# Kernel optimization log

Hardware: AMD Instinct MI355X
Metric: run time of the kernel (lower is better)

The kernel has to match this reference:

```python
import jax, jax.numpy as jnp
import numpy as np
import math

H = 8          # num_heads
DV = 1024      # dim_V
LN_EPS = 1e-5


def _layernorm(x, g, b):
    mu = jnp.mean(x, axis=-1, keepdims=True)
    var = jnp.mean(jnp.square(x - mu), axis=-1, keepdims=True)
    return (x - mu) * jax.lax.rsqrt(var + LN_EPS) * g + b


def setup_inputs() -> dict:
    key = jax.random.key(0)
    ks = jax.random.split(key, 12)
    B, NQ, NK, DQ, DK = 4, 2048, 2048, 1024, 1024
    s = 0.02
    return {
        "Q": jax.random.normal(ks[0], (B, NQ, DQ), jnp.float32),
        "K": jax.random.normal(ks[1], (B, NK, DK), jnp.float32),
        "Wq": jax.random.normal(ks[2], (DV, DQ), jnp.float32) * s,
        "bq": jnp.zeros((DV,), jnp.float32),
        "Wk": jax.random.normal(ks[3], (DV, DK), jnp.float32) * s,
        "bk": jnp.zeros((DV,), jnp.float32),
        "Wv": jax.random.normal(ks[4], (DV, DK), jnp.float32) * s,
        "bv": jnp.zeros((DV,), jnp.float32),
        "Wo": jax.random.normal(ks[5], (DV, DV), jnp.float32) * s,
        "bo": jnp.zeros((DV,), jnp.float32),
        "g0": jnp.ones((DV,), jnp.float32),
        "b0": jnp.zeros((DV,), jnp.float32),
        "g1": jnp.ones((DV,), jnp.float32),
        "b1": jnp.zeros((DV,), jnp.float32),
    }


def reference(Q, K, Wq, bq, Wk, bk, Wv, bv, Wo, bo, g0, b0, g1, b1):
    B, NQ, _ = Q.shape
    NK = K.shape[1]
    d = DV // H  # per-head dim
    # projections
    q = (Q @ Wq.T + bq).reshape(B, NQ, H, d)
    k = (K @ Wk.T + bk).reshape(B, NK, H, d)
    v = (K @ Wv.T + bv).reshape(B, NK, H, d)
    # attention per head (split along feature dim == head split in torch code)
    logits = jnp.einsum('bqhd,bkhd->bhqk', q, k) / math.sqrt(d)
    A = jax.nn.softmax(logits, axis=-1)
    o = q + jnp.einsum('bhqk,bkhd->bqhd', A, v)  # residual with projected Q
    O = o.reshape(B, NQ, DV)
    O = _layernorm(O, g0, b0)
    O = O + jax.nn.relu(O @ Wo.T + bo)
    O = _layernorm(O, g1, b1)
    return O
```

## Files before the change

### kernel.cpp

```cpp
#include <hip/hip_runtime.h>
#include <hip/hip_bf16.h>

typedef __bf16 bf16_t;
typedef __bf16 bf16x8 __attribute__((ext_vector_type(8)));
typedef __bf16 bf16x4 __attribute__((ext_vector_type(4)));
typedef float f32x4 __attribute__((ext_vector_type(4)));

#define B_DIM 4
#define NQ 2048
#define NK 2048
#define DMODEL 1024
#define NH 8
#define DHEAD 128

#define AS1 __attribute__((address_space(1)))
#define AS3 __attribute__((address_space(3)))

__device__ __forceinline__ void gl_lds16(const void* g, void* l) {
    __builtin_amdgcn_global_load_lds((const AS1 void*)g, (AS3 void*)l, 16, 0, 0);
}

struct CvtArgs {
    const float* s[6];
    bf16_t* d[6];
    int n[6];
};

__global__ __launch_bounds__(256) void cvt_k(CvtArgs a) {
    const int p = blockIdx.y;
    const float* s = a.s[p];
    bf16_t* d = a.d[p];
    const int n = a.n[p];
    const int stride = gridDim.x * 256 * 8;
    for (int i = (blockIdx.x * 256 + threadIdx.x) * 8; i < n; i += stride) {
        float4 x0 = *(const float4*)(s + i);
        float4 x1 = *(const float4*)(s + i + 4);
        bf16x8 o = {(bf16_t)x0.x, (bf16_t)x0.y, (bf16_t)x0.z, (bf16_t)x0.w,
                    (bf16_t)x1.x, (bf16_t)x1.y, (bf16_t)x1.z, (bf16_t)x1.w};
        *(bf16x8*)(d + i) = o;
    }
}

__global__ __launch_bounds__(256) void proj_k(
    const bf16_t* Qc, const bf16_t* Kc,
    const bf16_t* Wqc, const bf16_t* Wkc, const bf16_t* Wvc,
    const float* bq, const float* bk, const float* bv,
    bf16_t* qbb, bf16_t* kbb, bf16_t* vT)
{
    const int K = DMODEL, N = DMODEL;
    const int z = blockIdx.z;
    const bf16_t* A  = (z == 0) ? Qc : Kc;
    const bf16_t* Bw = (z == 0) ? Wqc : (z == 1) ? Wkc : Wvc;
    const float* bias = (z == 0) ? bq : (z == 1) ? bk : bv;
    bf16_t* Cb = (z == 0) ? qbb : (z == 1) ? kbb : vT;

    const int tid  = threadIdx.x;
    const int lane = tid & 63;
    const int wv   = tid >> 6;
    const int l16  = lane & 15;
    const int quad = (lane >> 4) & 3;
    const int kc4  = lane >> 4;
    const int wr   = wv >> 1, wc = wv & 1;
    const int rowBase = blockIdx.y * 128;
    const int colBase = blockIdx.x * 128;

    __shared__ bf16_t sA[4096];
    __shared__ bf16_t sB[4096];

    const bf16_t* gA = A + (size_t)(rowBase + wv * 32 + l16) * K + kc4 * 8;
    const bf16_t* gB = Bw + (size_t)(colBase + wv * 32 + l16) * K + kc4 * 8;
    bf16_t* lA0 = &sA[(wv * 2) * 512];
    bf16_t* lA1 = &sA[(wv * 2 + 1) * 512];
    bf16_t* lB0 = &sB[(wv * 2) * 512];
    bf16_t* lB1 = &sB[(wv * 2 + 1) * 512];

    const f32x4 fz = {0.f, 0.f, 0.f, 0.f};
    f32x4 acc[4][4];
#pragma unroll
    for (int i = 0; i < 4; i++)
#pragma unroll
        for (int j = 0; j < 4; j++) acc[i][j] = fz;

    for (int k0 = 0; k0 < K; k0 += 32) {
        gl_lds16(gA, lA0);
        gl_lds16(gA + (size_t)16 * K, lA1);
        gl_lds16(gB, lB0);
        gl_lds16(gB + (size_t)16 * K, lB1);
        gA += 32; gB += 32;
        __syncthreads();

        bf16x8 aF[4], bF[4];
#pragma unroll
        for (int mi = 0; mi < 4; mi++)
            aF[mi] = *(const bf16x8*)(&sA[(wr * 4 + mi) * 512 + (quad * 16 + l16) * 8]);
#pragma unroll
        for (int ni = 0; ni < 4; ni++)
            bF[ni] = *(const bf16x8*)(&sB[(wc * 4 + ni) * 512 + (quad * 16 + l16) * 8]);
#pragma unroll
        for (int mi = 0; mi < 4; mi++)
#pragma unroll
            for (int ni = 0; ni < 4; ni++)
                acc[mi][ni] = __builtin_amdgcn_mfma_f32_16x16x32_bf16(
                    aF[mi], bF[ni], acc[mi][ni], 0, 0, 0);
        __syncthreads();
    }

#pragma unroll
    for (int mi = 0; mi < 4; mi++) {
#pragma unroll
        for (int ni = 0; ni < 4; ni++) {
            int row0 = rowBase + wr * 64 + mi * 16 + quad * 4;
            int col  = colBase + wc * 64 + ni * 16 + l16;
            float bvv = bias[col];
            if (z != 2) {
#pragma unroll
                for (int r = 0; r < 4; r++)
                    Cb[(size_t)(row0 + r) * N + col] = (bf16_t)(acc[mi][ni][r] + bvv);
            } else {
                int b  = row0 >> 11;
                int n0 = row0 & 2047;
                int hh = col >> 7;
                int dd = col & 127;
                bf16x4 p = {(bf16_t)(acc[mi][ni][0] + bvv), (bf16_t)(acc[mi][ni][1] + bvv),
                            (bf16_t)(acc[mi][ni][2] + bvv), (bf16_t)(acc[mi][ni][3] + bvv)};
                *(bf16x4*)(Cb + (size_t)((b * NH + hh) * DHEAD + dd) * NK + n0) = p;
            }
        }
    }
}

__global__ __launch_bounds__(256) void gemm_wo(
    const bf16_t* __restrict__ A, const bf16_t* __restrict__ Bw,
    const float* __restrict__ bias, const float* resid, float* Cf, int M, int N, int K)
{
    const int tid  = threadIdx.x;
    const int lane = tid & 63;
    const int wv   = tid >> 6;
    const int l16  = lane & 15;
    const int quad = (lane >> 4) & 3;
    const int kc4  = lane >> 4;
    const int wr   = wv >> 1, wc = wv & 1;
    const int rowBase = blockIdx.y * 128;
    const int colBase = blockIdx.x * 128;

    __shared__ bf16_t sA[4096];
    __shared__ bf16_t sB[4096];

    const bf16_t* gA = A + (size_t)(rowBase + wv * 32 + l16) * K + kc4 * 8;
    const bf16_t* gB = Bw + (size_t)(colBase + wv * 32 + l16) * K + kc4 * 8;
    bf16_t* lA0 = &sA[(wv * 2) * 512];
    bf16_t* lA1 = &sA[(wv * 2 + 1) * 512];
    bf16_t* lB0 = &sB[(wv * 2) * 512];
    bf16_t* lB1 = &sB[(wv * 2 + 1) * 512];

    const f32x4 fz = {0.f, 0.f, 0.f, 0.f};
    f32x4 acc[4][4];
#pragma unroll
    for (int i = 0; i < 4; i++)
#pragma unroll
        for (int j = 0; j < 4; j++) acc[i][j] = fz;

    for (int k0 = 0; k0 < K; k0 += 32) {
        gl_lds16(gA, lA0);
        gl_lds16(gA + (size_t)16 * K, lA1);
        gl_lds16(gB, lB0);
        gl_lds16(gB + (size_t)16 * K, lB1);
        gA += 32; gB += 32;
        __syncthreads();

        bf16x8 aF[4], bF[4];
#pragma unroll
        for (int mi = 0; mi < 4; mi++)
            aF[mi] = *(const bf16x8*)(&sA[(wr * 4 + mi) * 512 + (quad * 16 + l16) * 8]);
#pragma unroll
        for (int ni = 0; ni < 4; ni++)
            bF[ni] = *(const bf16x8*)(&sB[(wc * 4 + ni) * 512 + (quad * 16 + l16) * 8]);
#pragma unroll
        for (int mi = 0; mi < 4; mi++)
#pragma unroll
            for (int ni = 0; ni < 4; ni++)
                acc[mi][ni] = __builtin_amdgcn_mfma_f32_16x16x32_bf16(
                    aF[mi], bF[ni], acc[mi][ni], 0, 0, 0);
        __syncthreads();
    }

#pragma unroll
    for (int mi = 0; mi < 4; mi++) {
#pragma unroll
        for (int ni = 0; ni < 4; ni++) {
            int row0 = rowBase + wr * 64 + mi * 16 + quad * 4;
            int col  = colBase + wc * 64 + ni * 16 + l16;
            float bvv = bias[col];
#pragma unroll
            for (int r = 0; r < 4; r++) {
                float v = acc[mi][ni][r] + bvv;
                v = v > 0.f ? v : 0.f;
                Cf[(size_t)(row0 + r) * N + col] =
                    resid[(size_t)(row0 + r) * N + col] + v;
            }
        }
    }
}

__global__ __launch_bounds__(256, 2) void attn_k(
    const bf16_t* __restrict__ qb, const bf16_t* __restrict__ kb,
    const bf16_t* __restrict__ vT, float* __restrict__ O)
{
    const int tid  = threadIdx.x;
    const int lane = tid & 63;
    const int wv   = tid >> 6;
    const int l16  = lane & 15;
    const int quad = (lane >> 4) & 3;
    const int bh   = blockIdx.x;
    const int b    = bh >> 3;
    const int h    = bh & 7;
    const int qt   = blockIdx.y * 128;
    const int qrow0 = b * NQ + qt + wv * 32;

    __shared__ bf16_t sK[2][8192];
    __shared__ bf16_t sV[2][8192];

    const bf16_t* gKb = kb + ((size_t)b * NK + l16) * DMODEL + h * DHEAD + quad * 8;
    const bf16_t* gVb = vT + ((size_t)bh * DHEAD + l16) * NK + quad * 8;

    auto stage = [&](int kt, int bufi) {
#pragma unroll
        for (int c = 0; c < 4; c++)
            gl_lds16(gKb + (size_t)(kt + wv * 16) * DMODEL + c * 32,
                     &sK[bufi][(wv * 4 + c) * 512]);
#pragma unroll
        for (int d2 = 0; d2 < 2; d2++) {
            const int dbi = wv * 2 + d2;
#pragma unroll
            for (int kc = 0; kc < 2; kc++)
                gl_lds16(gVb + (size_t)(dbi * 16) * NK + kt + kc * 32,
                         &sV[bufi][(dbi * 2 + kc) * 512]);
        }
    };

    stage(0, 0);

    bf16x8 qF[2][4];
#pragma unroll
    for (int qq = 0; qq < 2; qq++)
#pragma unroll
        for (int c = 0; c < 4; c++)
            qF[qq][c] = *(const bf16x8*)(qb + (size_t)(qrow0 + qq * 16 + l16) * DMODEL +
                                         h * DHEAD + c * 32 + quad * 8);

    const f32x4 fz = {0.f, 0.f, 0.f, 0.f};
    f32x4 accO[8][2];
#pragma unroll
    for (int db = 0; db < 8; db++)
#pragma unroll
        for (int qq = 0; qq < 2; qq++) accO[db][qq] = fz;
    float mq[2] = {-3e38f, -3e38f};
    float lq[2] = {0.f, 0.f};
    const float SC2 = 0.08838834764831845f * 1.44269504089f;

    const int qa   = (quad & 1) * 2;
    const int srcA = l16 + 16 * qa;
    const int srcB = srcA + 16;
    const bool hi  = (quad >> 1) != 0;

    __syncthreads();
    int cur = 0;

    for (int kt = 0; kt < NK; kt += 64) {
        if (kt + 64 < NK) stage(kt + 64, cur ^ 1);

        f32x4 S[4][2];
        __builtin_amdgcn_s_setprio(1);
#pragma unroll
        for (int kb4 = 0; kb4 < 4; kb4++) {
            S[kb4][0] = fz; S[kb4][1] = fz;
#pragma unroll
            for (int c = 0; c < 4; c++) {
                bf16x8 kF = *(const bf16x8*)(&sK[cur][(kb4 * 4 + c) * 512 + lane * 8]);
                S[kb4][0] = __builtin_amdgcn_mfma_f32_16x16x32_bf16(kF, qF[0][c], S[kb4][0], 0, 0, 0);
                S[kb4][1] = __builtin_amdgcn_mfma_f32_16x16x32_bf16(kF, qF[1][c], S[kb4][1], 0, 0, 0);
            }
        }
        __builtin_amdgcn_s_setprio(0);

        float alph[2];
#pragma unroll
        for (int qq = 0; qq < 2; qq++) {
            float mx = fmaxf(fmaxf(fmaxf(S[0][qq][0], S[0][qq][1]), fmaxf(S[0][qq][2], S[0][qq][3])),
                       fmaxf(fmaxf(S[1][qq][0], S[1][qq][1]), fmaxf(S[1][qq][2], S[1][qq][3])));
            mx = fmaxf(mx, fmaxf(fmaxf(fmaxf(S[2][qq][0], S[2][qq][1]), fmaxf(S[2][qq][2], S[2][qq][3])),
                           fmaxf(fmaxf(S[3][qq][0], S[3][qq][1]), fmaxf(S[3][qq][2], S[3][qq][3]))));
            mx = fmaxf(mx, __shfl_xor(mx, 16));
            mx = fmaxf(mx, __shfl_xor(mx, 32));
            float mn = fmaxf(mq[qq], mx);
            float al = exp2f((mq[qq] - mn) * SC2);
            mq[qq] = mn;
            float mc = mn * SC2;
            float sum = 0.f;
#pragma unroll
            for (int kb4 = 0; kb4 < 4; kb4++)
#pragma unroll
                for (int r = 0; r < 4; r++) {
                    float p = exp2f(fmaf(S[kb4][qq][r], SC2, -mc));
                    S[kb4][qq][r] = p;
                    sum += p;
                }
            lq[qq] = lq[qq] * al + sum;
            alph[qq] = al;
        }
#pragma unroll
        for (int db = 0; db < 8; db++)
#pragma unroll
            for (int qq = 0; qq < 2; qq++)
#pragma unroll
                for (int r = 0; r < 4; r++) accO[db][qq][r] *= alph[qq];

        uint2 pk[4][2];
#pragma unroll
        for (int kb4 = 0; kb4 < 4; kb4++)
#pragma unroll
            for (int qq = 0; qq < 2; qq++) {
                bf16x4 t = {(bf16_t)S[kb4][qq][0], (bf16_t)S[kb4][qq][1],
                            (bf16_t)S[kb4][qq][2], (bf16_t)S[kb4][qq][3]};
                pk[kb4][qq] = __builtin_bit_cast(uint2, t);
            }
        bf16x8 pF[2][2];
#pragma unroll
        for (int kc = 0; kc < 2; kc++)
#pragma unroll
            for (int qq = 0; qq < 2; qq++) {
                unsigned a0 = (unsigned)__shfl((int)pk[2 * kc][qq].x, srcA);
                unsigned b0 = (unsigned)__shfl((int)pk[2 * kc + 1][qq].x, srcA);
                unsigned a1 = (unsigned)__shfl((int)pk[2 * kc][qq].y, srcA);
                unsigned b1 = (unsigned)__shfl((int)pk[2 * kc + 1][qq].y, srcA);
                unsigned a2 = (unsigned)__shfl((int)pk[2 * kc][qq].x, srcB);
                unsigned b2 = (unsigned)__shfl((int)pk[2 * kc + 1][qq].x, srcB);
                unsigned a3 = (unsigned)__shfl((int)pk[2 * kc][qq].y, srcB);
                unsigned b3 = (unsigned)__shfl((int)pk[2 * kc + 1][qq].y, srcB);
                uint4 w = {hi ? b0 : a0, hi ? b1 : a1, hi ? b2 : a2, hi ? b3 : a3};
                pF[kc][qq] = __builtin_bit_cast(bf16x8, w);
            }

        __builtin_amdgcn_s_setprio(1);
#pragma unroll
        for (int kc = 0; kc < 2; kc++)
#pragma unroll
            for (int db = 0; db < 8; db++) {
                bf16x8 vF = *(const bf16x8*)(&sV[cur][(db * 2 + kc) * 512 + lane * 8]);
                accO[db][0] = __builtin_amdgcn_mfma_f32_16x16x32_bf16(vF, pF[kc][0], accO[db][0], 0, 0, 0);
                accO[db][1] = __builtin_amdgcn_mfma_f32_16x16x32_bf16(vF, pF[kc][1], accO[db][1], 0, 0, 0);
            }
        __builtin_amdgcn_s_setprio(0);

        __syncthreads();
        cur ^= 1;
    }

    float inv[2];
#pragma unroll
    for (int qq = 0; qq < 2; qq++) {
        float s = lq[qq];
        s += __shfl_xor(s, 16);
        s += __shfl_xor(s, 32);
        inv[qq] = 1.0f / s;
    }

#pragma unroll
    for (int qq = 0; qq < 2; qq++) {
        const int grow = qrow0 + qq * 16 + l16;
#pragma unroll
        for (int db = 0; db < 8; db++) {
            const int gcol = h * DHEAD + db * 16 + quad * 4;
            bf16x4 qr = *(const bf16x4*)(qb + (size_t)grow * DMODEL + gcol);
            f32x4 o;
#pragma unroll
            for (int r = 0; r < 4; r++)
                o[r] = accO[db][qq][r] * inv[qq] + (float)qr[r];
            *(f32x4*)(O + (size_t)grow * DMODEL + gcol) = o;
        }
    }
}

__global__ __launch_bounds__(256) void ln_k(
    const float* __restrict__ X, const float* __restrict__ g,
    const float* __restrict__ bta, float* __restrict__ Yf, bf16_t* Yb)
{
    const int row = blockIdx.x;
    const int t = threadIdx.x;
    float4 x = *(const float4*)(X + (size_t)row * DMODEL + t * 4);
    float s  = x.x + x.y + x.z + x.w;
    float sq = x.x * x.x + x.y * x.y + x.z * x.z + x.w * x.w;
#pragma unroll
    for (int o = 1; o < 64; o <<= 1) {
        s  += __shfl_xor(s, o);
        sq += __shfl_xor(sq, o);
    }
    __shared__ float ls[8];
    int w = t >> 6, ln = t & 63;
    if (ln == 0) { ls[w] = s; ls[4 + w] = sq; }
    __syncthreads();
    s  = ls[0] + ls[1] + ls[2] + ls[3];
    sq = ls[4] + ls[5] + ls[6] + ls[7];
    float mu  = s * (1.f / DMODEL);
    float var = sq * (1.f / DMODEL) - mu * mu;
    float rs  = rsqrtf(var + 1e-5f);
    float4 gv = *(const float4*)(g + t * 4);
    float4 bv = *(const float4*)(bta + t * 4);
    float4 y;
    y.x = (x.x - mu) * rs * gv.x + bv.x;
    y.y = (x.y - mu) * rs * gv.y + bv.y;
    y.z = (x.z - mu) * rs * gv.z + bv.z;
    y.w = (x.w - mu) * rs * gv.w + bv.w;
    *(float4*)(Yf + (size_t)row * DMODEL + t * 4) = y;
    if (Yb) {
        bf16x4 yb = {(bf16_t)y.x, (bf16_t)y.y, (bf16_t)y.z, (bf16_t)y.w};
        *(bf16x4*)(Yb + (size_t)row * DMODEL + t * 4) = yb;
    }
}

extern "C" void kernel_launch(void* const* d_in, const int* in_sizes, int n_in,
                              void* d_out, int out_size, void* d_ws, size_t ws_size,
                              hipStream_t stream)
{
    const float* Q  = (const float*)d_in[0];
    const float* Kx = (const float*)d_in[1];
    const float* Wq = (const float*)d_in[2];
    const float* bq = (const float*)d_in[3];
    const float* Wk = (const float*)d_in[4];
    const float* bk = (const float*)d_in[5];
    const float* Wv = (const float*)d_in[6];
    const float* bv = (const float*)d_in[7];
    const float* Wo = (const float*)d_in[8];
    const float* bo = (const float*)d_in[9];
    const float* g0 = (const float*)d_in[10];
    const float* b0 = (const float*)d_in[11];
    const float* g1 = (const float*)d_in[12];
    const float* b1 = (const float*)d_in[13];
    float* out = (float*)d_out;

    char* ws = (char*)d_ws;
    bf16_t* Qc  = (bf16_t*)(ws);
    bf16_t* Kc  = (bf16_t*)(ws + 16777216);
    bf16_t* Wqc = (bf16_t*)(ws + 33554432);
    bf16_t* Wkc = (bf16_t*)(ws + 35651584);
    bf16_t* Wvc = (bf16_t*)(ws + 37748736);
    bf16_t* Woc = (bf16_t*)(ws + 39845888);
    bf16_t* qbb = (bf16_t*)(ws + 41943040);
    bf16_t* kbb = (bf16_t*)(ws + 58720256);
    bf16_t* vT  = (bf16_t*)(ws + 75497472);
    float*  Obuf = (float*)(ws + 92274688);
    float*  Lf  = (float*)(ws);
    bf16_t* Lb  = kbb;

    CvtArgs ca;
    ca.s[0] = Q;  ca.d[0] = Qc;  ca.n[0] = B_DIM * NQ * DMODEL;
    ca.s[1] = Kx; ca.d[1] = Kc;  ca.n[1] = B_DIM * NK * DMODEL;
    ca.s[2] = Wq; ca.d[2] = Wqc; ca.n[2] = DMODEL * DMODEL;
    ca.s[3] = Wk; ca.d[3] = Wkc; ca.n[3] = DMODEL * DMODEL;
    ca.s[4] = Wv; ca.d[4] = Wvc; ca.n[4] = DMODEL * DMODEL;
    ca.s[5] = Wo; ca.d[5] = Woc; ca.n[5] = DMODEL * DMODEL;
    cvt_k<<<dim3(512, 6), 256, 0, stream>>>(ca);

    const int M = B_DIM * NQ;

    proj_k<<<dim3(DMODEL / 128, M / 128, 3), 256, 0, stream>>>(
        Qc, Kc, Wqc, Wkc, Wvc, bq, bk, bv, qbb, kbb, vT);

    attn_k<<<dim3(B_DIM * NH, NQ / 128), 256, 0, stream>>>(qbb, kbb, vT, Obuf);

    ln_k<<<dim3(M), 256, 0, stream>>>(Obuf, g0, b0, Lf, Lb);

    gemm_wo<<<dim3(DMODEL / 128, M / 128), 256, 0, stream>>>(
        Lb, Woc, bo, Lf, Lf, M, DMODEL, DMODEL);

    ln_k<<<dim3(M), 256, 0, stream>>>(Lf, g1, b1, out, nullptr);
}
```

Before: 441.9 us.

## Software-pipeline QK^T of next tile with softmax and PV of current tile

Restructures the flash-attention loop so the QK^T MFMAs for tile t+1 are issued right after the PV MFMAs of tile t, using two ping-pong score register sets. K and V staging are split so the next K tile is prefetched one step further ahead, and V is staged after the barrier. The aim is to overlap the exp/shuffle softmax work with matrix-core work and to hide load latency better. In exchange it roughly doubles the live score registers, which risks spills or lower occupancy under launch bounds 256,2.

Result: no change. 439.4 us (-0.6%).

```diff
diff --git a/kernel.cpp b/kernel.cpp
--- a/kernel.cpp
+++ b/kernel.cpp
@@ -216,6 +216,7 @@
     const int h    = bh & 7;
     const int qt   = blockIdx.y * 128;
     const int qrow0 = b * NQ + qt + wv * 32;
+    const int NKT  = NK / 64;
 
     __shared__ bf16_t sK[2][8192];
     __shared__ bf16_t sV[2][8192];
@@ -223,11 +224,15 @@
     const bf16_t* gKb = kb + ((size_t)b * NK + l16) * DMODEL + h * DHEAD + quad * 8;
     const bf16_t* gVb = vT + ((size_t)bh * DHEAD + l16) * NK + quad * 8;
 
-    auto stage = [&](int kt, int bufi) {
+    auto stageK = [&](int tt, int bufi) {
+        const int kt = tt * 64;
 #pragma unroll
         for (int c = 0; c < 4; c++)
             gl_lds16(gKb + (size_t)(kt + wv * 16) * DMODEL + c * 32,
                      &sK[bufi][(wv * 4 + c) * 512]);
+    };
+    auto stageV = [&](int tt, int bufi) {
+        const int kt = tt * 64;
 #pragma unroll
         for (int d2 = 0; d2 < 2; d2++) {
             const int dbi = wv * 2 + d2;
@@ -238,7 +243,9 @@
         }
     };
 
-    stage(0, 0);
+    stageK(0, 0);
+    stageV(0, 0);
+    stageK(1, 1);
 
     bf16x8 qF[2][4];
 #pragma unroll
@@ -263,33 +270,33 @@
     const int srcB = srcA + 16;
     const bool hi  = (quad >> 1) != 0;
 
+    f32x4 SA[4][2], SB[4][2];
+
     __syncthreads();
-    int cur = 0;
-
-    for (int kt = 0; kt < NK; kt += 64) {
-        if (kt + 64 < NK) stage(kt + 64, cur ^ 1);
-
-        f32x4 S[4][2];
-        __builtin_amdgcn_s_setprio(1);
-#pragma unroll
-        for (int kb4 = 0; kb4 < 4; kb4++) {
-            S[kb4][0] = fz; S[kb4][1] = fz;
-#pragma unroll
-            for (int c = 0; c < 4; c++) {
-                bf16x8 kF = *(const bf16x8*)(&sK[cur][(kb4 * 4 + c) * 512 + lane * 8]);
-                S[kb4][0] = __builtin_amdgcn_mfma_f32_16x16x32_bf16(kF, qF[0][c], S[kb4][0], 0, 0, 0);
-                S[kb4][1] = __builtin_amdgcn_mfma_f32_16x16x32_bf16(kF, qF[1][c], S[kb4][1], 0, 0, 0);
-            }
-        }
-        __builtin_amdgcn_s_setprio(0);
+
+#pragma unroll
+    for (int kb4 = 0; kb4 < 4; kb4++) {
+        SA[kb4][0] = fz; SA[kb4][1] = fz;
+#pragma unroll
+        for (int c = 0; c < 4; c++) {
+            bf16x8 kF = *(const bf16x8*)(&sK[0][(kb4 * 4 + c) * 512 + lane * 8]);
+            SA[kb4][0] = __builtin_amdgcn_mfma_f32_16x16x32_bf16(kF, qF[0][c], SA[kb4][0], 0, 0, 0);
+            SA[kb4][1] = __builtin_amdgcn_mfma_f32_16x16x32_bf16(kF, qF[1][c], SA[kb4][1], 0, 0, 0);
+        }
+    }
+    __syncthreads();
+    stageV(1, 1);
+
+    auto body = [&](int t, f32x4 (&Scur)[4][2], f32x4 (&Snxt)[4][2], int CB) {
+        if (t + 2 < NKT) stageK(t + 2, CB);
 
         float alph[2];
 #pragma unroll
         for (int qq = 0; qq < 2; qq++) {
-            float mx = fmaxf(fmaxf(fmaxf(S[0][qq][0], S[0][qq][1]), fmaxf(S[0][qq][2], S[0][qq][3])),
-                       fmaxf(fmaxf(S[1][qq][0], S[1][qq][1]), fmaxf(S[1][qq][2], S[1][qq][3])));
-            mx = fmaxf(mx, fmaxf(fmaxf(fmaxf(S[2][qq][0], S[2][qq][1]), fmaxf(S[2][qq][2], S[2][qq][3])),
-                           fmaxf(fmaxf(S[3][qq][0], S[3][qq][1]), fmaxf(S[3][qq][2], S[3][qq][3]))));
+            float mx = fmaxf(fmaxf(fmaxf(Scur[0][qq][0], Scur[0][qq][1]), fmaxf(Scur[0][qq][2], Scur[0][qq][3])),
+                       fmaxf(fmaxf(Scur[1][qq][0], Scur[1][qq][1]), fmaxf(Scur[1][qq][2], Scur[1][qq][3])));
+            mx = fmaxf(mx, fmaxf(fmaxf(fmaxf(Scur[2][qq][0], Scur[2][qq][1]), fmaxf(Scur[2][qq][2], Scur[2][qq][3])),
+                           fmaxf(fmaxf(Scur[3][qq][0], Scur[3][qq][1]), fmaxf(Scur[3][qq][2], Scur[3][qq][3]))));
             mx = fmaxf(mx, __shfl_xor(mx, 16));
             mx = fmaxf(mx, __shfl_xor(mx, 32));
             float mn = fmaxf(mq[qq], mx);
@@ -301,8 +308,8 @@
             for (int kb4 = 0; kb4 < 4; kb4++)
 #pragma unroll
                 for (int r = 0; r < 4; r++) {
-                    float p = exp2f(fmaf(S[kb4][qq][r], SC2, -mc));
-                    S[kb4][qq][r] = p;
+                    float p = exp2f(fmaf(Scur[kb4][qq][r], SC2, -mc));
+                    Scur[kb4][qq][r] = p;
                     sum += p;
                 }
             lq[qq] = lq[qq] * al + sum;
@@ -320,9 +327,9 @@
         for (int kb4 = 0; kb4 < 4; kb4++)
 #pragma unroll
             for (int qq = 0; qq < 2; qq++) {
-                bf16x4 t = {(bf16_t)S[kb4][qq][0], (bf16_t)S[kb4][qq][1],
-                            (bf16_t)S[kb4][qq][2], (bf16_t)S[kb4][qq][3]};
-                pk[kb4][qq] = __builtin_bit_cast(uint2, t);
+                bf16x4 tt = {(bf16_t)Scur[kb4][qq][0], (bf16_t)Scur[kb4][qq][1],
+                             (bf16_t)Scur[kb4][qq][2], (bf16_t)Scur[kb4][qq][3]};
+                pk[kb4][qq] = __builtin_bit_cast(uint2, tt);
             }
         bf16x8 pF[2][2];
 #pragma unroll
@@ -346,14 +353,31 @@
         for (int kc = 0; kc < 2; kc++)
 #pragma unroll
             for (int db = 0; db < 8; db++) {
-                bf16x8 vF = *(const bf16x8*)(&sV[cur][(db * 2 + kc) * 512 + lane * 8]);
+                bf16x8 vF = *(const bf16x8*)(&sV[CB][(db * 2 + kc) * 512 + lane * 8]);
                 accO[db][0] = __builtin_amdgcn_mfma_f32_16x16x32_bf16(vF, pF[kc][0], accO[db][0], 0, 0, 0);
                 accO[db][1] = __builtin_amdgcn_mfma_f32_16x16x32_bf16(vF, pF[kc][1], accO[db][1], 0, 0, 0);
             }
+        if (t + 1 < NKT) {
+#pragma unroll
+            for (int kb4 = 0; kb4 < 4; kb4++) {
+                Snxt[kb4][0] = fz; Snxt[kb4][1] = fz;
+#pragma unroll
+                for (int c = 0; c < 4; c++) {
+                    bf16x8 kF = *(const bf16x8*)(&sK[CB ^ 1][(kb4 * 4 + c) * 512 + lane * 8]);
+                    Snxt[kb4][0] = __builtin_amdgcn_mfma_f32_16x16x32_bf16(kF, qF[0][c], Snxt[kb4][0], 0, 0, 0);
+                    Snxt[kb4][1] = __builtin_amdgcn_mfma_f32_16x16x32_bf16(kF, qF[1][c], Snxt[kb4][1], 0, 0, 0);
+                }
+            }
+        }
         __builtin_amdgcn_s_setprio(0);
 
         __syncthreads();
-        cur ^= 1;
+        if (t + 2 < NKT) stageV(t + 2, CB);
+    };
+
+    for (int t = 0; t < NKT; t += 2) {
+        body(t,     SA, SB, 0);
+        body(t + 1, SB, SA, 1);
     }
 
     float inv[2];
```

## Use 8 waves of 16 query rows in attention, add lazy softmax rescale

Applied to the files above, without the earlier changes.

The attention kernel now launches 512 threads per block, so each of the 8 waves owns 16 query rows instead of 32. This halves the per-wave accumulator and score registers, and the K/V staging is spread across more waves, aiming for higher occupancy and latency hiding. It also adds a lazy rescale: the running max and the accumulator rescale are only updated when some lane's max grows by more than a threshold. That removes rescale multiplies but lets exponent values reach up to 2^8 before rescaling. Each K/V tile loaded into LDS is now reused by fewer query rows per wave, and the MFMA work per wave per tile is smaller.

Measured after the change: 430.5 us. 2.6% less time.

```diff
diff --git a/kernel.cpp b/kernel.cpp
--- a/kernel.cpp
+++ b/kernel.cpp
@@ -202,7 +202,7 @@
     }
 }
 
-__global__ __launch_bounds__(256, 2) void attn_k(
+__global__ __launch_bounds__(512, 4) void attn_k(
     const bf16_t* __restrict__ qb, const bf16_t* __restrict__ kb,
     const bf16_t* __restrict__ vT, float* __restrict__ O)
 {
@@ -215,7 +215,8 @@
     const int b    = bh >> 3;
     const int h    = bh & 7;
     const int qt   = blockIdx.y * 128;
-    const int qrow0 = b * NQ + qt + wv * 32;
+    const int qrow = b * NQ + qt + wv * 16;
+    const int NKT  = NK / 64;
 
     __shared__ bf16_t sK[2][8192];
     __shared__ bf16_t sV[2][8192];
@@ -223,39 +224,38 @@
     const bf16_t* gKb = kb + ((size_t)b * NK + l16) * DMODEL + h * DHEAD + quad * 8;
     const bf16_t* gVb = vT + ((size_t)bh * DHEAD + l16) * NK + quad * 8;
 
-    auto stage = [&](int kt, int bufi) {
-#pragma unroll
-        for (int c = 0; c < 4; c++)
-            gl_lds16(gKb + (size_t)(kt + wv * 16) * DMODEL + c * 32,
-                     &sK[bufi][(wv * 4 + c) * 512]);
-#pragma unroll
-        for (int d2 = 0; d2 < 2; d2++) {
-            const int dbi = wv * 2 + d2;
-#pragma unroll
-            for (int kc = 0; kc < 2; kc++)
-                gl_lds16(gVb + (size_t)(dbi * 16) * NK + kt + kc * 32,
-                         &sV[bufi][(dbi * 2 + kc) * 512]);
+    auto stage = [&](int tt, int bufi) {
+        const int kt = tt * 64;
+#pragma unroll
+        for (int j = 0; j < 2; j++) {
+            const int f = wv * 2 + j;
+            const int kbi = f >> 2, c = f & 3;
+            gl_lds16(gKb + (size_t)(kt + kbi * 16) * DMODEL + c * 32,
+                     &sK[bufi][f * 512]);
+        }
+#pragma unroll
+        for (int j = 0; j < 2; j++) {
+            const int g = wv * 2 + j;
+            const int dbi = g >> 1, kc = g & 1;
+            gl_lds16(gVb + (size_t)(dbi * 16) * NK + kt + kc * 32,
+                     &sV[bufi][g * 512]);
         }
     };
 
     stage(0, 0);
 
-    bf16x8 qF[2][4];
-#pragma unroll
-    for (int qq = 0; qq < 2; qq++)
-#pragma unroll
-        for (int c = 0; c < 4; c++)
-            qF[qq][c] = *(const bf16x8*)(qb + (size_t)(qrow0 + qq * 16 + l16) * DMODEL +
-                                         h * DHEAD + c * 32 + quad * 8);
+    bf16x8 qF[4];
+#pragma unroll
+    for (int c = 0; c < 4; c++)
+        qF[c] = *(const bf16x8*)(qb + (size_t)(qrow + l16) * DMODEL +
+                                 h * DHEAD + c * 32 + quad * 8);
 
     const f32x4 fz = {0.f, 0.f, 0.f, 0.f};
-    f32x4 accO[8][2];
-#pragma unroll
-    for (int db = 0; db < 8; db++)
-#pragma unroll
-        for (int qq = 0; qq < 2; qq++) accO[db][qq] = fz;
-    float mq[2] = {-3e38f, -3e38f};
-    float lq[2] = {0.f, 0.f};
+    f32x4 accO[8];
+#pragma unroll
+    for (int db = 0; db < 8; db++) accO[db] = fz;
+    float mq = -3e38f;
+    float lq = 0.f;
     const float SC2 = 0.08838834764831845f * 1.44269504089f;
 
     const int qa   = (quad & 1) * 2;
@@ -266,80 +266,74 @@
     __syncthreads();
     int cur = 0;
 
-    for (int kt = 0; kt < NK; kt += 64) {
-        if (kt + 64 < NK) stage(kt + 64, cur ^ 1);
-
-        f32x4 S[4][2];
+    for (int t = 0; t < NKT; t++) {
+        if (t + 1 < NKT) stage(t + 1, cur ^ 1);
+
+        f32x4 S[4];
         __builtin_amdgcn_s_setprio(1);
 #pragma unroll
         for (int kb4 = 0; kb4 < 4; kb4++) {
-            S[kb4][0] = fz; S[kb4][1] = fz;
+            S[kb4] = fz;
 #pragma unroll
             for (int c = 0; c < 4; c++) {
                 bf16x8 kF = *(const bf16x8*)(&sK[cur][(kb4 * 4 + c) * 512 + lane * 8]);
-                S[kb4][0] = __builtin_amdgcn_mfma_f32_16x16x32_bf16(kF, qF[0][c], S[kb4][0], 0, 0, 0);
-                S[kb4][1] = __builtin_amdgcn_mfma_f32_16x16x32_bf16(kF, qF[1][c], S[kb4][1], 0, 0, 0);
+                S[kb4] = __builtin_amdgcn_mfma_f32_16x16x32_bf16(kF, qF[c], S[kb4], 0, 0, 0);
             }
         }
         __builtin_amdgcn_s_setprio(0);
 
-        float alph[2];
-#pragma unroll
-        for (int qq = 0; qq < 2; qq++) {
-            float mx = fmaxf(fmaxf(fmaxf(S[0][qq][0], S[0][qq][1]), fmaxf(S[0][qq][2], S[0][qq][3])),
-                       fmaxf(fmaxf(S[1][qq][0], S[1][qq][1]), fmaxf(S[1][qq][2], S[1][qq][3])));
-            mx = fmaxf(mx, fmaxf(fmaxf(fmaxf(S[2][qq][0], S[2][qq][1]), fmaxf(S[2][qq][2], S[2][qq][3])),
-                           fmaxf(fmaxf(S[3][qq][0], S[3][qq][1]), fmaxf(S[3][qq][2], S[3][qq][3]))));
-            mx = fmaxf(mx, __shfl_xor(mx, 16));
-            mx = fmaxf(mx, __shfl_xor(mx, 32));
-            float mn = fmaxf(mq[qq], mx);
-            float al = exp2f((mq[qq] - mn) * SC2);
-            mq[qq] = mn;
-            float mc = mn * SC2;
-            float sum = 0.f;
-#pragma unroll
-            for (int kb4 = 0; kb4 < 4; kb4++)
-#pragma unroll
-                for (int r = 0; r < 4; r++) {
-                    float p = exp2f(fmaf(S[kb4][qq][r], SC2, -mc));
-                    S[kb4][qq][r] = p;
-                    sum += p;
-                }
-            lq[qq] = lq[qq] * al + sum;
-            alph[qq] = al;
-        }
-#pragma unroll
-        for (int db = 0; db < 8; db++)
-#pragma unroll
-            for (int qq = 0; qq < 2; qq++)
-#pragma unroll
-                for (int r = 0; r < 4; r++) accO[db][qq][r] *= alph[qq];
-
-        uint2 pk[4][2];
+        float mx = fmaxf(fmaxf(fmaxf(S[0][0], S[0][1]), fmaxf(S[0][2], S[0][3])),
+                   fmaxf(fmaxf(S[1][0], S[1][1]), fmaxf(S[1][2], S[1][3])));
+        mx = fmaxf(mx, fmaxf(fmaxf(fmaxf(S[2][0], S[2][1]), fmaxf(S[2][2], S[2][3])),
+                       fmaxf(fmaxf(S[3][0], S[3][1]), fmaxf(S[3][2], S[3][3]))));
+        mx = fmaxf(mx, __shfl_xor(mx, 16));
+        mx = fmaxf(mx, __shfl_xor(mx, 32));
+        const bool need = !__all((mx - mq) * SC2 <= 8.f);
+        float al = 1.f;
+        if (need) {
+            float mn = fmaxf(mq, mx);
+            al = exp2f((mq - mn) * SC2);
+            mq = mn;
+        }
+        const float mc = mq * SC2;
+        float sum = 0.f;
 #pragma unroll
         for (int kb4 = 0; kb4 < 4; kb4++)
 #pragma unroll
-            for (int qq = 0; qq < 2; qq++) {
-                bf16x4 t = {(bf16_t)S[kb4][qq][0], (bf16_t)S[kb4][qq][1],
-                            (bf16_t)S[kb4][qq][2], (bf16_t)S[kb4][qq][3]};
-                pk[kb4][qq] = __builtin_bit_cast(uint2, t);
+            for (int r = 0; r < 4; r++) {
+                float p = exp2f(fmaf(S[kb4][r], SC2, -mc));
+                S[kb4][r] = p;
+                sum += p;
             }
-        bf16x8 pF[2][2];
-#pragma unroll
-        for (int kc = 0; kc < 2; kc++)
-#pragma unroll
-            for (int qq = 0; qq < 2; qq++) {
-                unsigned a0 = (unsigned)__shfl((int)pk[2 * kc][qq].x, srcA);
-                unsigned b0 = (unsigned)__shfl((int)pk[2 * kc + 1][qq].x, srcA);
-                unsigned a1 = (unsigned)__shfl((int)pk[2 * kc][qq].y, srcA);
-                unsigned b1 = (unsigned)__shfl((int)pk[2 * kc + 1][qq].y, srcA);
-                unsigned a2 = (unsigned)__shfl((int)pk[2 * kc][qq].x, srcB);
-                unsigned b2 = (unsigned)__shfl((int)pk[2 * kc + 1][qq].x, srcB);
-                unsigned a3 = (unsigned)__shfl((int)pk[2 * kc][qq].y, srcB);
-                unsigned b3 = (unsigned)__shfl((int)pk[2 * kc + 1][qq].y, srcB);
-                uint4 w = {hi ? b0 : a0, hi ? b1 : a1, hi ? b2 : a2, hi ? b3 : a3};
-                pF[kc][qq] = __builtin_bit_cast(bf16x8, w);
-            }
+        lq = lq * al + sum;
+        if (need) {
+#pragma unroll
+            for (int db = 0; db < 8; db++)
+#pragma unroll
+                for (int r = 0; r < 4; r++) accO[db][r] *= al;
+        }
+
+        uint2 pk[4];
+#pragma unroll
+        for (int kb4 = 0; kb4 < 4; kb4++) {
+            bf16x4 tt = {(bf16_t)S[kb4][0], (bf16_t)S[kb4][1],
+                         (bf16_t)S[kb4][2], (bf16_t)S[kb4][3]};
+            pk[kb4] = __builtin_bit_cast(uint2, tt);
+        }
+        bf16x8 pF[2];
+#pragma unroll
+        for (int kc = 0; kc < 2; kc++) {
+            unsigned a0 = (unsigned)__shfl((int)pk[2 * kc].x, srcA);
+            unsigned b0 = (unsigned)__shfl((int)pk[2 * kc + 1].x, srcA);
+            unsigned a1 = (unsigned)__shfl((int)pk[2 * kc].y, srcA);
+            unsigned b1 = (unsigned)__shfl((int)pk[2 * kc + 1].y, srcA);
+            unsigned a2 = (unsigned)__shfl((int)pk[2 * kc].x, srcB);
+            unsigned b2 = (unsigned)__shfl((int)pk[2 * kc + 1].x, srcB);
+            unsigned a3 = (unsigned)__shfl((int)pk[2 * kc].y, srcB);
+            unsigned b3 = (unsigned)__shfl((int)pk[2 * kc + 1].y, srcB);
+            uint4 w = {hi ? b0 : a0, hi ? b1 : a1, hi ? b2 : a2, hi ? b3 : a3};
+            pF[kc] = __builtin_bit_cast(bf16x8, w);
+        }
 
         __builtin_amdgcn_s_setprio(1);
 #pragma unroll
@@ -347,8 +341,7 @@
 #pragma unroll
             for (int db = 0; db < 8; db++) {
                 bf16x8 vF = *(const bf16x8*)(&sV[cur][(db * 2 + kc) * 512 + lane * 8]);
-                accO[db][0] = __builtin_amdgcn_mfma_f32_16x16x32_bf16(vF, pF[kc][0], accO[db][0], 0, 0, 0);
-                accO[db][1] = __builtin_amdgcn_mfma_f32_16x16x32_bf16(vF, pF[kc][1], accO[db][1], 0, 0, 0);
+                accO[db] = __builtin_amdgcn_mfma_f32_16x16x32_bf16(vF, pF[kc], accO[db], 0, 0, 0);
             }
         __builtin_amdgcn_s_setprio(0);
 
@@ -356,28 +349,21 @@
         cur ^= 1;
     }
 
-    float inv[2];
-#pragma unroll
-    for (int qq = 0; qq < 2; qq++) {
-        float s = lq[qq];
-        s += __shfl_xor(s, 16);
-        s += __shfl_xor(s, 32);
-        inv[qq] = 1.0f / s;
-    }
-
-#pragma unroll
-    for (int qq = 0; qq < 2; qq++) {
-        const int grow = qrow0 + qq * 16 + l16;
-#pragma unroll
-        for (int db = 0; db < 8; db++) {
-            const int gcol = h * DHEAD + db * 16 + quad * 4;
-            bf16x4 qr = *(const bf16x4*)(qb + (size_t)grow * DMODEL + gcol);
-            f32x4 o;
-#pragma unroll
-            for (int r = 0; r < 4; r++)
-                o[r] = accO[db][qq][r] * inv[qq] + (float)qr[r];
-            *(f32x4*)(O + (size_t)grow * DMODEL + gcol) = o;
-        }
+    float s = lq;
+    s += __shfl_xor(s, 16);
+    s += __shfl_xor(s, 32);
+    const float inv = 1.0f / s;
+
+    const int grow = qrow + l16;
+#pragma unroll
+    for (int db = 0; db < 8; db++) {
+        const int gcol = h * DHEAD + db * 16 + quad * 4;
+        bf16x4 qr = *(const bf16x4*)(qb + (size_t)grow * DMODEL + gcol);
+        f32x4 o;
+#pragma unroll
+        for (int r = 0; r < 4; r++)
+            o[r] = accO[db][r] * inv + (float)qr[r];
+        *(f32x4*)(O + (size_t)grow * DMODEL + gcol) = o;
     }
 }
 
@@ -466,7 +452,7 @@
     proj_k<<<dim3(DMODEL / 128, M / 128, 3), 256, 0, stream>>>(
         Qc, Kc, Wqc, Wkc, Wvc, bq, bk, bv, qbb, kbb, vT);
 
-    attn_k<<<dim3(B_DIM * NH, NQ / 128), 256, 0, stream>>>(qbb, kbb, vT, Obuf);
+    attn_k<<<dim3(B_DIM * NH, NQ / 128), 512, 0, stream>>>(qbb, kbb, vT, Obuf);
 
     ln_k<<<dim3(M), 256, 0, stream>>>(Obuf, g0, b0, Lf, Lb);
 
```

## Split attention over key halves with lazy rescaling and fused combine-layernorm

Applied to the files above, without the earlier changes.

The attention kernel now splits the key sequence into two halves along a new grid dimension. Each block runs 8 waves over 256 queries, so one staged K/V tile is shared by twice as many queries, and the block writes unnormalised partial outputs plus per-row max and sum. A new ln0 kernel merges the two partials with softmax weights, adds the Q residual and applies the first layernorm, which removes the separate Obuf normalisation pass. Online-softmax rescaling of the accumulator is skipped unless the running max rises by more than a threshold, which cuts per-tile VALU work. The costs are extra partial-output traffic and register pressure under the tighter 512x4 launch bounds, which could cause spills.

Result: slower. 548.1 us (+24.0%).

```diff
diff --git a/kernel.cpp b/kernel.cpp
--- a/kernel.cpp
+++ b/kernel.cpp
@@ -202,9 +202,10 @@
     }
 }
 
-__global__ __launch_bounds__(256, 2) void attn_k(
+__global__ __launch_bounds__(512, 4) void attn_k(
     const bf16_t* __restrict__ qb, const bf16_t* __restrict__ kb,
-    const bf16_t* __restrict__ vT, float* __restrict__ O)
+    const bf16_t* __restrict__ vT, float* __restrict__ O0,
+    float* __restrict__ O1, float* __restrict__ ml)
 {
     const int tid  = threadIdx.x;
     const int lane = tid & 63;
@@ -214,27 +215,33 @@
     const int bh   = blockIdx.x;
     const int b    = bh >> 3;
     const int h    = bh & 7;
-    const int qt   = blockIdx.y * 128;
+    const int qt   = blockIdx.y * 256;
+    const int ks   = blockIdx.z;
+    const int kbase = ks * (NK / 2);
     const int qrow0 = b * NQ + qt + wv * 32;
+    const int NIT  = (NK / 2) / 64;
 
     __shared__ bf16_t sK[2][8192];
     __shared__ bf16_t sV[2][8192];
 
-    const bf16_t* gKb = kb + ((size_t)b * NK + l16) * DMODEL + h * DHEAD + quad * 8;
-    const bf16_t* gVb = vT + ((size_t)bh * DHEAD + l16) * NK + quad * 8;
-
-    auto stage = [&](int kt, int bufi) {
-#pragma unroll
-        for (int c = 0; c < 4; c++)
-            gl_lds16(gKb + (size_t)(kt + wv * 16) * DMODEL + c * 32,
-                     &sK[bufi][(wv * 4 + c) * 512]);
-#pragma unroll
-        for (int d2 = 0; d2 < 2; d2++) {
-            const int dbi = wv * 2 + d2;
-#pragma unroll
-            for (int kc = 0; kc < 2; kc++)
-                gl_lds16(gVb + (size_t)(dbi * 16) * NK + kt + kc * 32,
-                         &sV[bufi][(dbi * 2 + kc) * 512]);
+    const bf16_t* gKb = kb + ((size_t)(b * NK + kbase) + l16) * DMODEL + h * DHEAD + quad * 8;
+    const bf16_t* gVb = vT + ((size_t)bh * DHEAD + l16) * NK + kbase + quad * 8;
+
+    auto stage = [&](int tt, int bufi) {
+        const int kt = tt * 64;
+#pragma unroll
+        for (int j = 0; j < 2; j++) {
+            const int f = wv * 2 + j;
+            const int kbi = f >> 2, c = f & 3;
+            gl_lds16(gKb + (size_t)(kt + kbi * 16) * DMODEL + c * 32,
+                     &sK[bufi][f * 512]);
+        }
+#pragma unroll
+        for (int j = 0; j < 2; j++) {
+            const int g = wv * 2 + j;
+            const int dbi = g >> 1, kc = g & 1;
+            gl_lds16(gVb + (size_t)(dbi * 16) * NK + kt + kc * 32,
+                     &sV[bufi][g * 512]);
         }
     };
 
@@ -266,8 +273,8 @@
     __syncthreads();
     int cur = 0;
 
-    for (int kt = 0; kt < NK; kt += 64) {
-        if (kt + 64 < NK) stage(kt + 64, cur ^ 1);
+    for (int t = 0; t < NIT; t++) {
+        if (t + 1 < NIT) stage(t + 1, cur ^ 1);
 
         f32x4 S[4][2];
         __builtin_amdgcn_s_setprio(1);
@@ -283,7 +290,6 @@
         }
         __builtin_amdgcn_s_setprio(0);
 
-        float alph[2];
 #pragma unroll
         for (int qq = 0; qq < 2; qq++) {
             float mx = fmaxf(fmaxf(fmaxf(S[0][qq][0], S[0][qq][1]), fmaxf(S[0][qq][2], S[0][qq][3])),
@@ -292,10 +298,14 @@
                            fmaxf(fmaxf(S[3][qq][0], S[3][qq][1]), fmaxf(S[3][qq][2], S[3][qq][3]))));
             mx = fmaxf(mx, __shfl_xor(mx, 16));
             mx = fmaxf(mx, __shfl_xor(mx, 32));
-            float mn = fmaxf(mq[qq], mx);
-            float al = exp2f((mq[qq] - mn) * SC2);
-            mq[qq] = mn;
-            float mc = mn * SC2;
+            const bool need = !__all((mx - mq[qq]) * SC2 <= 8.f);
+            float al = 1.f;
+            if (need) {
+                float mn = fmaxf(mq[qq], mx);
+                al = exp2f((mq[qq] - mn) * SC2);
+                mq[qq] = mn;
+            }
+            const float mc = mq[qq] * SC2;
             float sum = 0.f;
 #pragma unroll
             for (int kb4 = 0; kb4 < 4; kb4++)
@@ -306,23 +316,22 @@
                     sum += p;
                 }
             lq[qq] = lq[qq] * al + sum;
-            alph[qq] = al;
-        }
-#pragma unroll
-        for (int db = 0; db < 8; db++)
-#pragma unroll
-            for (int qq = 0; qq < 2; qq++)
-#pragma unroll
-                for (int r = 0; r < 4; r++) accO[db][qq][r] *= alph[qq];
+            if (need) {
+#pragma unroll
+                for (int db = 0; db < 8; db++)
+#pragma unroll
+                    for (int r = 0; r < 4; r++) accO[db][qq][r] *= al;
+            }
+        }
 
         uint2 pk[4][2];
 #pragma unroll
         for (int kb4 = 0; kb4 < 4; kb4++)
 #pragma unroll
             for (int qq = 0; qq < 2; qq++) {
-                bf16x4 t = {(bf16_t)S[kb4][qq][0], (bf16_t)S[kb4][qq][1],
-                            (bf16_t)S[kb4][qq][2], (bf16_t)S[kb4][qq][3]};
-                pk[kb4][qq] = __builtin_bit_cast(uint2, t);
+                bf16x4 tt = {(bf16_t)S[kb4][qq][0], (bf16_t)S[kb4][qq][1],
+                             (bf16_t)S[kb4][qq][2], (bf16_t)S[kb4][qq][3]};
+                pk[kb4][qq] = __builtin_bit_cast(uint2, tt);
             }
         bf16x8 pF[2][2];
 #pragma unroll
@@ -356,29 +365,79 @@
         cur ^= 1;
     }
 
-    float inv[2];
+    float* Op = ks ? O1 : O0;
 #pragma unroll
     for (int qq = 0; qq < 2; qq++) {
         float s = lq[qq];
         s += __shfl_xor(s, 16);
         s += __shfl_xor(s, 32);
-        inv[qq] = 1.0f / s;
-    }
-
-#pragma unroll
-    for (int qq = 0; qq < 2; qq++) {
         const int grow = qrow0 + qq * 16 + l16;
 #pragma unroll
         for (int db = 0; db < 8; db++) {
             const int gcol = h * DHEAD + db * 16 + quad * 4;
-            bf16x4 qr = *(const bf16x4*)(qb + (size_t)grow * DMODEL + gcol);
-            f32x4 o;
-#pragma unroll
-            for (int r = 0; r < 4; r++)
-                o[r] = accO[db][qq][r] * inv[qq] + (float)qr[r];
-            *(f32x4*)(O + (size_t)grow * DMODEL + gcol) = o;
-        }
-    }
+            *(f32x4*)(Op + (size_t)grow * DMODEL + gcol) = accO[db][qq];
+        }
+        if (quad == 0) {
+            float2 v = {mq[qq], s};
+            *(float2*)(ml + (((size_t)ks * NH + h) * (B_DIM * NQ) + grow) * 2) = v;
+        }
+    }
+}
+
+__global__ __launch_bounds__(256) void ln0_k(
+    const float* O0, const float* O1,
+    const float* __restrict__ ml, const bf16_t* __restrict__ qb,
+    const float* __restrict__ g, const float* __restrict__ bta,
+    float* Yf, bf16_t* Yb)
+{
+    const int row = blockIdx.x;
+    const int t = threadIdx.x;
+    const int hh = t >> 5;
+    const int M = B_DIM * NQ;
+    const float SC2 = 0.08838834764831845f * 1.44269504089f;
+    float2 mlA = *(const float2*)(ml + ((size_t)hh * M + row) * 2);
+    float2 mlB = *(const float2*)(ml + ((size_t)(NH + hh) * M + row) * 2);
+    float Mx = fmaxf(mlA.x, mlB.x);
+    float wA = exp2f((mlA.x - Mx) * SC2);
+    float wB = exp2f((mlB.x - Mx) * SC2);
+    float inv = 1.f / (mlA.y * wA + mlB.y * wB);
+    wA *= inv; wB *= inv;
+
+    float4 a0 = *(const float4*)(O0 + (size_t)row * DMODEL + t * 4);
+    float4 a1 = *(const float4*)(O1 + (size_t)row * DMODEL + t * 4);
+    bf16x4 qr = *(const bf16x4*)(qb + (size_t)row * DMODEL + t * 4);
+    float4 x;
+    x.x = a0.x * wA + a1.x * wB + (float)qr[0];
+    x.y = a0.y * wA + a1.y * wB + (float)qr[1];
+    x.z = a0.z * wA + a1.z * wB + (float)qr[2];
+    x.w = a0.w * wA + a1.w * wB + (float)qr[3];
+
+    float s  = x.x + x.y + x.z + x.w;
+    float sq = x.x * x.x + x.y * x.y + x.z * x.z + x.w * x.w;
+#pragma unroll
+    for (int o = 1; o < 64; o <<= 1) {
+        s  += __shfl_xor(s, o);
+        sq += __shfl_xor(sq, o);
+    }
+    __shared__ float ls[8];
+    int w = t >> 6, ln = t & 63;
+    if (ln == 0) { ls[w] = s; ls[4 + w] = sq; }
+    __syncthreads();
+    s  = ls[0] + ls[1] + ls[2] + ls[3];
+    sq = ls[4] + ls[5] + ls[6] + ls[7];
+    float mu  = s * (1.f / DMODEL);
+    float var = sq * (1.f / DMODEL) - mu * mu;
+    float rs  = rsqrtf(var + 1e-5f);
+    float4 gv = *(const float4*)(g + t * 4);
+    float4 bv = *(const float4*)(bta + t * 4);
+    float4 y;
+    y.x = (x.x - mu) * rs * gv.x + bv.x;
+    y.y = (x.y - mu) * rs * gv.y + bv.y;
+    y.z = (x.z - mu) * rs * gv.z + bv.z;
+    y.w = (x.w - mu) * rs * gv.w + bv.w;
+    *(float4*)(Yf + (size_t)row * DMODEL + t * 4) = y;
+    bf16x4 yb = {(bf16_t)y.x, (bf16_t)y.y, (bf16_t)y.z, (bf16_t)y.w};
+    *(bf16x4*)(Yb + (size_t)row * DMODEL + t * 4) = yb;
 }
 
 __global__ __launch_bounds__(256) void ln_k(
@@ -449,6 +508,8 @@
     bf16_t* kbb = (bf16_t*)(ws + 58720256);
     bf16_t* vT  = (bf16_t*)(ws + 75497472);
     float*  Obuf = (float*)(ws + 92274688);
+    float*  Opart1 = (float*)(ws);
+    float*  mlbuf  = (float*)(ws + 33554432);
     float*  Lf  = (float*)(ws);
     bf16_t* Lb  = kbb;
 
@@ -466,9 +527,10 @@
     proj_k<<<dim3(DMODEL / 128, M / 128, 3), 256, 0, stream>>>(
         Qc, Kc, Wqc, Wkc, Wvc, bq, bk, bv, qbb, kbb, vT);
 
-    attn_k<<<dim3(B_DIM * NH, NQ / 128), 256, 0, stream>>>(qbb, kbb, vT, Obuf);
-
-    ln_k<<<dim3(M), 256, 0, stream>>>(Obuf, g0, b0, Lf, Lb);
+    attn_k<<<dim3(B_DIM * NH, NQ / 256, 2), 512, 0, stream>>>(
+        qbb, kbb, vT, Obuf, Opart1, mlbuf);
+
+    ln0_k<<<dim3(M), 256, 0, stream>>>(Obuf, Opart1, mlbuf, qbb, g0, b0, Lf, Lb);
 
     gemm_wo<<<dim3(DMODEL / 128, M / 128), 256, 0, stream>>>(
         Lb, Woc, bo, Lf, Lf, M, DMODEL, DMODEL);
```
